# Kernel optimization log

Measured on AMD Instinct MI355X. Metric: run time of the kernel, lower is better.

Reference implementation:

```python
import jax, jax.numpy as jnp
import numpy as np

D_MODEL = 2048
N_HEADS = 16
HEAD_DIM = D_MODEL // N_HEADS


def setup_inputs() -> dict:
    key = jax.random.key(0)
    ks = jax.random.split(key, 5)
    s = 0.02
    return {
        "x": jax.random.normal(ks[0], (4, 2048, D_MODEL), dtype=jnp.float32),
        "w_qkv": jax.random.normal(ks[1], (D_MODEL, 3 * D_MODEL), dtype=jnp.float32) * s,
        "b_qkv": jnp.zeros((3 * D_MODEL,), dtype=jnp.float32),
        "w_out": jax.random.normal(ks[2], (D_MODEL, D_MODEL), dtype=jnp.float32) * s,
        "b_out": jnp.zeros((D_MODEL,), dtype=jnp.float32),
    }


def reference(x, w_qkv, b_qkv, w_out, b_out):
    B, T, C = x.shape
    qkv = x @ w_qkv + b_qkv  # [B,T,3C]
    q, k, v = jnp.split(qkv, 3, axis=-1)
    # [B,T,C] -> [B,H,T,hd]
    def to_heads(t):
        return t.reshape(B, T, N_HEADS, HEAD_DIM).transpose(0, 2, 1, 3)
    q, k, v = to_heads(q), to_heads(k), to_heads(v)
    scale = 1.0 / jnp.sqrt(jnp.asarray(HEAD_DIM, dtype=x.dtype))
    attn = jnp.einsum("bhqd,bhkd->bhqk", q, k) * scale
    causal = jnp.tril(jnp.ones((T, T), dtype=bool))
    attn = jnp.where(causal[None, None], attn, jnp.asarray(-jnp.inf, dtype=attn.dtype))
    attn = jax.nn.softmax(attn, axis=-1)
    out = jnp.einsum("bhqk,bhkd->bhqd", attn, v)
    out = out.transpose(0, 2, 1, 3).reshape(B, T, C)
    return out @ w_out + b_out
```

## Files before the change

### kernel.cpp

```cpp
#include <hip/hip_runtime.h>
#include <hip/hip_bf16.h>

#define DEVFN static __device__ __forceinline__

typedef __attribute__((ext_vector_type(8))) __bf16 bf16x8;
typedef __attribute__((ext_vector_type(4))) float f32x4;

#define MFMA16(a, b, c) __builtin_amdgcn_mfma_f32_16x16x32_bf16(a, b, c, 0, 0, 0)

DEVFN void gload16(const void* g, void* l) {
  __builtin_amdgcn_global_load_lds((const __attribute__((address_space(1))) void*)g,
                                   (__attribute__((address_space(3))) void*)l, 16, 0, 0);
}

DEVFN void vwait8() { asm volatile("s_waitcnt vmcnt(8)" ::: "memory"); __builtin_amdgcn_sched_barrier(0); }
DEVFN void vwait4() { asm volatile("s_waitcnt vmcnt(4)" ::: "memory"); __builtin_amdgcn_sched_barrier(0); }
DEVFN void vwait0() { asm volatile("s_waitcnt vmcnt(0)" ::: "memory"); __builtin_amdgcn_sched_barrier(0); }
DEVFN void bar()    { __builtin_amdgcn_s_barrier(); }
DEVFN void barsched() { __builtin_amdgcn_s_barrier(); __builtin_amdgcn_sched_barrier(0); }

__global__ __launch_bounds__(256) void cvt_f32_bf16(const float* __restrict__ in,
                                                    __bf16* __restrict__ out) {
  size_t i = ((size_t)blockIdx.x * 256 + threadIdx.x) * 8;
  f32x4 a = *(const f32x4*)(in + i);
  f32x4 b = *(const f32x4*)(in + i + 4);
  bf16x8 u;
  u[0] = (__bf16)a[0]; u[1] = (__bf16)a[1]; u[2] = (__bf16)a[2]; u[3] = (__bf16)a[3];
  u[4] = (__bf16)b[0]; u[5] = (__bf16)b[1]; u[6] = (__bf16)b[2]; u[7] = (__bf16)b[3];
  *(bf16x8*)(out + i) = u;
}

__global__ __launch_bounds__(256) void transpose_w(const float* __restrict__ in,
                                                   __bf16* __restrict__ out,
                                                   int K, int N) {
  __shared__ float tile[32][33];
  const int t = threadIdx.x, tx = t & 31, ty = t >> 5;
  const int n0 = blockIdx.x * 32, k0 = blockIdx.y * 32;
#pragma unroll
  for (int r = 0; r < 4; r++)
    tile[ty + r * 8][tx] = in[(size_t)(k0 + ty + r * 8) * N + n0 + tx];
  __syncthreads();
#pragma unroll
  for (int r = 0; r < 4; r++)
    out[(size_t)(n0 + ty + r * 8) * K + k0 + tx] = (__bf16)tile[tx][ty + r * 8];
}

__global__ __launch_bounds__(256) void transpose_v(const __bf16* __restrict__ in,
                                                   __bf16* __restrict__ out) {
  __shared__ __bf16 tile[64][72];
  const int bh = blockIdx.z;
  const int t0 = blockIdx.x * 64, d0 = blockIdx.y * 64;
  const int tid = threadIdx.x;
  const int r = tid >> 3, c8 = (tid & 7) * 8;
  const __bf16* ip = in + (size_t)bh * 2048 * 128;
#pragma unroll
  for (int i = 0; i < 2; i++)
    *(bf16x8*)&tile[i * 32 + r][c8] =
        *(const bf16x8*)(ip + (size_t)(t0 + i * 32 + r) * 128 + d0 + c8);
  __syncthreads();
  __bf16* op = out + (size_t)bh * 2048 * 128;
#pragma unroll
  for (int i = 0; i < 2; i++) {
    const int dd = i * 32 + r;
    bf16x8 v;
#pragma unroll
    for (int j = 0; j < 8; j++) v[j] = tile[c8 + j][dd];
    *(bf16x8*)(op + (size_t)(d0 + dd) * 2048 + t0 + c8) = v;
  }
}

#define QK_SCALE 0.12751745f

DEVFN void stage_tile(const __bf16* gx, size_t Kst, int t, __bf16* ldst,
                      int rr, int gsw, int w) {
#pragma unroll
  for (int j = 0; j < 4; j++)
    gload16(gx + (size_t)(j * 64 + rr) * Kst + (size_t)t * 64 + gsw,
            ldst + j * 4096 + w * 512);
}

DEVFN void stage_chunk(const __bf16* gx, size_t Kst, int t, __bf16* ldst, int j,
                       int rr, int gsw, int w) {
  gload16(gx + (size_t)(j * 64 + rr) * Kst + (size_t)t * 64 + gsw,
          ldst + j * 4096 + w * 512);
}

DEVFN void tile_step(__bf16* la, __bf16* lb, f32x4 (&acc)[8][4],
                     const __bf16* ga, const __bf16* gb, size_t Kst, int t, int NT,
                     int rr, int gsw, int w, int wr, int wc, int lg, int li) {
  bf16x8 a[4][2], bl[2][2], br[2][2];
  const int sa = li & 7;
  const int arow = wr * 128 + li;
  const int brow = wc * 64 + li;
  const bool pf = (t + 2 < NT);

#pragma unroll
  for (int mi = 0; mi < 4; mi++)
#pragma unroll
    for (int ks = 0; ks < 2; ks++)
      a[mi][ks] = *(const bf16x8*)&la[(arow + mi * 16) * 64 + (((ks * 4 + lg) ^ sa) * 8)];
#pragma unroll
  for (int ni = 0; ni < 2; ni++)
#pragma unroll
    for (int ks = 0; ks < 2; ks++)
      bl[ni][ks] = *(const bf16x8*)&lb[(brow + ni * 16) * 64 + (((ks * 4 + lg) ^ sa) * 8)];
  bar();
  __builtin_amdgcn_s_setprio(1);
#pragma unroll
  for (int mi = 0; mi < 4; mi++)
#pragma unroll
    for (int ni = 0; ni < 2; ni++)
#pragma unroll
      for (int ks = 0; ks < 2; ks++)
        acc[mi][ni] = MFMA16(a[mi][ks], bl[ni][ks], acc[mi][ni]);
  __builtin_amdgcn_s_setprio(0);
  barsched();

#pragma unroll
  for (int ni = 0; ni < 2; ni++)
#pragma unroll
    for (int ks = 0; ks < 2; ks++)
      br[ni][ks] = *(const bf16x8*)&lb[(brow + (ni + 2) * 16) * 64 + (((ks * 4 + lg) ^ sa) * 8)];
  if (pf) {
    stage_chunk(ga, Kst, t + 2, la, 0, rr, gsw, w);
    stage_chunk(ga, Kst, t + 2, la, 2, rr, gsw, w);
  }
  bar();
  __builtin_amdgcn_s_setprio(1);
#pragma unroll
  for (int mi = 0; mi < 4; mi++)
#pragma unroll
    for (int ni = 0; ni < 2; ni++)
#pragma unroll
      for (int ks = 0; ks < 2; ks++)
        acc[mi][ni + 2] = MFMA16(a[mi][ks], br[ni][ks], acc[mi][ni + 2]);
  __builtin_amdgcn_s_setprio(0);
  barsched();

#pragma unroll
  for (int mi = 0; mi < 4; mi++)
#pragma unroll
    for (int ks = 0; ks < 2; ks++)
      a[mi][ks] = *(const bf16x8*)&la[(arow + (mi + 4) * 16) * 64 + (((ks * 4 + lg) ^ sa) * 8)];
  if (pf) {
    stage_chunk(gb, Kst, t + 2, lb, 0, rr, gsw, w);
    stage_chunk(gb, Kst, t + 2, lb, 1, rr, gsw, w);
  }
  bar();
  __builtin_amdgcn_s_setprio(1);
#pragma unroll
  for (int mi = 0; mi < 4; mi++)
#pragma unroll
    for (int ni = 0; ni < 2; ni++)
#pragma unroll
      for (int ks = 0; ks < 2; ks++)
        acc[mi + 4][ni] = MFMA16(a[mi][ks], bl[ni][ks], acc[mi + 4][ni]);
  __builtin_amdgcn_s_setprio(0);
  barsched();

  if (pf) {
    stage_chunk(gb, Kst, t + 2, lb, 2, rr, gsw, w);
    stage_chunk(gb, Kst, t + 2, lb, 3, rr, gsw, w);
    stage_chunk(ga, Kst, t + 2, la, 1, rr, gsw, w);
    stage_chunk(ga, Kst, t + 2, la, 3, rr, gsw, w);
  }
  __builtin_amdgcn_s_setprio(1);
#pragma unroll
  for (int mi = 0; mi < 4; mi++)
#pragma unroll
    for (int ni = 0; ni < 2; ni++)
#pragma unroll
      for (int ks = 0; ks < 2; ks++)
        acc[mi + 4][ni + 2] = MFMA16(a[mi][ks], br[ni][ks], acc[mi + 4][ni + 2]);
  __builtin_amdgcn_s_setprio(0);

  if (pf) vwait8(); else vwait0();
  bar();
}

template <int MODE>
__global__ __launch_bounds__(512, 2) void gemm256(
    const __bf16* __restrict__ A, const __bf16* __restrict__ Bt,
    const float* __restrict__ bias, int K, int Ncols,
    __bf16* __restrict__ qo, __bf16* __restrict__ ko, __bf16* __restrict__ vo,
    float* __restrict__ outf) {
  __shared__ __align__(16) __bf16 lds[65536];
  const int tid = threadIdx.x;
  const int w = tid >> 6, lane = tid & 63;
  const int wr = w >> 2, wc = w & 3;
  const int lg = lane >> 4, li = lane & 15;
  const int nbx = gridDim.x;
  const int orig = (int)blockIdx.y * nbx + (int)blockIdx.x;
  const int x = orig & 7, i = orig >> 3;
  const int xc = x & 1, xr = x >> 1;
  const int hw = nbx >> 1;
  const int band = i >> 5;
  const int j = i & 31;
  const size_t n0 = (size_t)(xc * hw + band * 4 + (j & 3)) * 256;
  const size_t m0 = (size_t)(xr * 8 + (j >> 2)) * 256;
  const int rr = tid >> 3;
  const int gsw = ((tid & 7) ^ (rr & 7)) * 8;
  const __bf16* ga = A + m0 * K;
  const __bf16* gb = Bt + n0 * K;
  const int NT = K >> 6;

  __bf16* la0 = lds;
  __bf16* la1 = lds + 16384;
  __bf16* lb0 = lds + 32768;
  __bf16* lb1 = lds + 49152;

  f32x4 acc[8][4] = {};

  stage_tile(ga, K, 0, la0, rr, gsw, w);
  stage_tile(gb, K, 0, lb0, rr, gsw, w);
  stage_tile(ga, K, 1, la1, rr, gsw, w);
  stage_tile(gb, K, 1, lb1, rr, gsw, w);
  vwait8();
  bar();

  for (int t = 0; t < NT; t += 2) {
    tile_step(la0, lb0, acc, ga, gb, K, t,     NT, rr, gsw, w, wr, wc, lg, li);
    tile_step(la1, lb1, acc, ga, gb, K, t + 1, NT, rr, gsw, w, wr, wc, lg, li);
  }

  if (MODE == 0) {
    const int which = (int)(n0 >> 11);
    const int b = (int)(m0 >> 11);
    __bf16* outp = (which == 0) ? qo : ((which == 1) ? ko : vo);
    const float scale = (which == 0) ? QK_SCALE : 1.0f;
#pragma unroll
    for (int ni = 0; ni < 4; ni++) {
      const int ncol = (int)n0 + wc * 64 + ni * 16 + li;
      const float bv = bias[ncol];
      const int h = (ncol & 2047) >> 7;
      const int d = ncol & 127;
      const size_t base = (size_t)(b * 16 + h) * (2048 * 128) + d;
#pragma unroll
      for (int mi = 0; mi < 8; mi++)
#pragma unroll
        for (int r = 0; r < 4; r++) {
          const int tt = ((int)m0 + wr * 128 + mi * 16 + lg * 4 + r) & 2047;
          outp[base + (size_t)tt * 128] = (__bf16)((acc[mi][ni][r] + bv) * scale);
        }
    }
  } else {
#pragma unroll
    for (int ni = 0; ni < 4; ni++) {
      const int ncol = (int)n0 + wc * 64 + ni * 16 + li;
      const float bv = bias[ncol];
#pragma unroll
      for (int mi = 0; mi < 8; mi++)
#pragma unroll
        for (int r = 0; r < 4; r++) {
          const size_t mrow = m0 + wr * 128 + mi * 16 + lg * 4 + r;
          outf[mrow * Ncols + ncol] = acc[mi][ni][r] + bv;
        }
    }
  }
}

DEVFN void attn_stageK(const __bf16* const (&ksrc)[4], int k0, __bf16* Kl, int w) {
#pragma unroll
  for (int i = 0; i < 4; i++)
    gload16(ksrc[i] + (size_t)k0 * 128, Kl + i * 2048 + w * 512);
}
DEVFN void attn_stageV(const __bf16* const (&vsrc)[4], int k0, __bf16* Vl, int w) {
#pragma unroll
  for (int i = 0; i < 4; i++)
    gload16(vsrc[i] + k0, Vl + i * 2048 + w * 512);
}

template <bool DIAG>
DEVFN void attn_tile(int kt, int n, int q0, int w, int lg, int li,
                     const __bf16* const (&ksrc)[4], const __bf16* const (&vsrc)[4],
                     __bf16* Kl, __bf16* Vl, __bf16* Pl,
                     const bf16x8 (&qf)[2][4], f32x4 (&o)[2][8],
                     float (&mrow)[2][4], float (&lrow)[2][4]) {
  const int k0 = kt * 64;
  const bool more = (kt + 1 < n);

  vwait4();
  barsched();

  f32x4 s[2][4] = {};
#pragma unroll
  for (int kk = 0; kk < 4; kk++) {
    bf16x8 bk[4];
#pragma unroll
    for (int ni = 0; ni < 4; ni++) {
      const int key = ni * 16 + li;
      bk[ni] = *(const bf16x8*)&Kl[key * 128 + ((kk * 32 + lg * 8) ^ ((key & 7) << 3))];
    }
#pragma unroll
    for (int mi = 0; mi < 2; mi++)
#pragma unroll
      for (int ni = 0; ni < 4; ni++)
        s[mi][ni] = MFMA16(qf[mi][kk], bk[ni], s[mi][ni]);
  }
  barsched();
  if (more) attn_stageK(ksrc, k0 + 64, Kl, w);

#pragma unroll
  for (int mi = 0; mi < 2; mi++) {
#pragma unroll
    for (int r = 0; r < 4; r++) {
      const int prow = w * 32 + mi * 16 + lg * 4 + r;
      float vals[4];
#pragma unroll
      for (int ni = 0; ni < 4; ni++) {
        float x = s[mi][ni][r];
        if (DIAG) {
          if ((k0 + ni * 16 + li) > (q0 + prow)) x = -1e30f;
        }
        vals[ni] = x;
      }
      float vmax = fmaxf(fmaxf(vals[0], vals[1]), fmaxf(vals[2], vals[3]));
      vmax = fmaxf(vmax, __shfl_xor(vmax, 1));
      vmax = fmaxf(vmax, __shfl_xor(vmax, 2));
      vmax = fmaxf(vmax, __shfl_xor(vmax, 4));
      vmax = fmaxf(vmax, __shfl_xor(vmax, 8));
      float mref = mrow[mi][r];
      if (vmax - mref > 8.0f) {
        const float sc = __builtin_amdgcn_exp2f(mref - vmax);
        lrow[mi][r] *= sc;
#pragma unroll
        for (int nd = 0; nd < 8; nd++) o[mi][nd][r] *= sc;
        mrow[mi][r] = vmax;
        mref = vmax;
      }
      float ps = 0.f;
#pragma unroll
      for (int ni = 0; ni < 4; ni++) {
        const float p = __builtin_amdgcn_exp2f(vals[ni] - mref);
        ps += p;
        Pl[prow * 72 + ni * 16 + li] = (__bf16)p;
      }
      ps += __shfl_xor(ps, 1);
      ps += __shfl_xor(ps, 2);
      ps += __shfl_xor(ps, 4);
      ps += __shfl_xor(ps, 8);
      lrow[mi][r] += ps;
    }
  }

  if (more) vwait4(); else vwait0();
  barsched();

#pragma unroll
  for (int kk = 0; kk < 2; kk++) {
    bf16x8 pf[2];
#pragma unroll
    for (int mi = 0; mi < 2; mi++)
      pf[mi] = *(const bf16x8*)&Pl[(w * 32 + mi * 16 + li) * 72 + kk * 32 + lg * 8];
#pragma unroll
    for (int nd = 0; nd < 8; nd++) {
      const int d = nd * 16 + li;
      const int swd = ((d ^ (d >> 3)) & 7) << 3;
      bf16x8 vf = *(const bf16x8*)&Vl[d * 64 + ((kk * 32 + lg * 8) ^ swd)];
#pragma unroll
      for (int mi = 0; mi < 2; mi++)
        o[mi][nd] = MFMA16(pf[mi], vf, o[mi][nd]);
    }
  }
  barsched();
  if (more) attn_stageV(vsrc, k0 + 64, Vl, w);
}

DEVFN void attn_run(int qt, int bh, int w, int lg, int li,
                    const __bf16* qp, __bf16* ob,
                    const __bf16* const (&ksrc)[4], const __bf16* const (&vsrc)[4],
                    __bf16* Kl, __bf16* Vl, __bf16* Pl) {
  const int q0 = qt * 128;
  bf16x8 qf[2][4];
#pragma unroll
  for (int mi = 0; mi < 2; mi++)
#pragma unroll
    for (int kk = 0; kk < 4; kk++)
      qf[mi][kk] = *(const bf16x8*)(qp + (size_t)(q0 + w * 32 + mi * 16 + li) * 128 + kk * 32 + lg * 8);

  f32x4 o[2][8] = {};
  float mrow[2][4], lrow[2][4];
#pragma unroll
  for (int mi = 0; mi < 2; mi++)
#pragma unroll
    for (int r = 0; r < 4; r++) { mrow[mi][r] = -1e30f; lrow[mi][r] = 0.f; }

  const int n = 2 * qt + 2;
  attn_stageK(ksrc, 0, Kl, w);
  attn_stageV(vsrc, 0, Vl, w);

  for (int kt = 0; kt < n - 2; kt++)
    attn_tile<false>(kt, n, q0, w, lg, li, ksrc, vsrc, Kl, Vl, Pl, qf, o, mrow, lrow);
  attn_tile<true>(n - 2, n, q0, w, lg, li, ksrc, vsrc, Kl, Vl, Pl, qf, o, mrow, lrow);
  attn_tile<true>(n - 1, n, q0, w, lg, li, ksrc, vsrc, Kl, Vl, Pl, qf, o, mrow, lrow);

  const int b = bh >> 4, h = bh & 15;
#pragma unroll
  for (int mi = 0; mi < 2; mi++) {
    float inv[4];
#pragma unroll
    for (int r = 0; r < 4; r++) inv[r] = 1.0f / lrow[mi][r];
#pragma unroll
    for (int nd = 0; nd < 8; nd++)
#pragma unroll
      for (int r = 0; r < 4; r++)
        ob[(size_t)(b * 2048 + q0 + w * 32 + mi * 16 + lg * 4 + r) * 2048 + h * 128 + nd * 16 + li]
            = (__bf16)(o[mi][nd][r] * inv[r]);
  }
}

__global__ __launch_bounds__(256, 2) void attn_fwd(
    const __bf16* __restrict__ qb, const __bf16* __restrict__ kb,
    const __bf16* __restrict__ vtb, __bf16* __restrict__ ob) {
  __shared__ __align__(16) __bf16 Kl[64 * 128];
  __shared__ __align__(16) __bf16 Vl[128 * 64];
  __shared__ __align__(16) __bf16 Pl[128 * 72];
  const int orig = (int)blockIdx.y * 8 + (int)blockIdx.x;
  const int swz = (orig & 7) * 64 + (orig >> 3);
  const int bx = swz & 7;
  const int bh = swz >> 3;
  const int tid = threadIdx.x;
  const int w = tid >> 6, l = tid & 63;
  const int lg = l >> 4, li = l & 15;
  const __bf16* qp = qb + (size_t)bh * (2048 * 128);
  const __bf16* kp = kb + (size_t)bh * (2048 * 128);
  const __bf16* vtp = vtb + (size_t)bh * (2048 * 128);

  const __bf16* ksrc[4];
  const __bf16* vsrc[4];
#pragma unroll
  for (int i = 0; i < 4; i++) {
    const int key = i * 16 + w * 4 + lg;
    ksrc[i] = kp + (size_t)key * 128 + 8 * (li ^ (key & 7));
    const int d = i * 32 + (tid >> 3);
    const int g = (tid & 7) ^ ((d ^ (d >> 3)) & 7);
    vsrc[i] = vtp + (size_t)d * 2048 + g * 8;
  }

  attn_run(15 - bx, bh, w, lg, li, qp, ob, ksrc, vsrc, Kl, Vl, Pl);
  attn_run(bx,      bh, w, lg, li, qp, ob, ksrc, vsrc, Kl, Vl, Pl);
}

extern "C" void kernel_launch(void* const* d_in, const int* in_sizes, int n_in,
                              void* d_out, int out_size, void* d_ws, size_t ws_size,
                              hipStream_t stream) {
  (void)in_sizes; (void)n_in; (void)out_size; (void)ws_size;
  const float* x     = (const float*)d_in[0];
  const float* w_qkv = (const float*)d_in[1];
  const float* b_qkv = (const float*)d_in[2];
  const float* w_out = (const float*)d_in[3];
  const float* b_out = (const float*)d_in[4];
  float* out = (float*)d_out;
  char* ws = (char*)d_ws;

  __bf16* xb    = (__bf16*)(ws + 0);
  __bf16* wqkvT = (__bf16*)(ws + 33554432);
  __bf16* qbuf  = (__bf16*)(ws + 58720256);
  __bf16* kbuf  = (__bf16*)(ws + 92274688);
  __bf16* vbuf  = (__bf16*)(ws + 125829120);
  __bf16* woutT = (__bf16*)(ws + 159383552);

  cvt_f32_bf16<<<8192, 256, 0, stream>>>(x, xb);
  transpose_w<<<dim3(192, 64), 256, 0, stream>>>(w_qkv, wqkvT, 2048, 6144);
  transpose_w<<<dim3(64, 64), 256, 0, stream>>>(w_out, woutT, 2048, 2048);
  gemm256<0><<<dim3(24, 32), 512, 0, stream>>>(xb, wqkvT, b_qkv, 2048, 6144,
                                               qbuf, kbuf, vbuf, nullptr);
  transpose_v<<<dim3(32, 2, 64), 256, 0, stream>>>(vbuf, xb);
  attn_fwd<<<dim3(8, 64), 256, 0, stream>>>(qbuf, kbuf, xb, vbuf);
  gemm256<1><<<dim3(8, 32), 512, 0, stream>>>(vbuf, woutT, b_out, 2048, 2048,
                                              nullptr, nullptr, nullptr, out);
}
```

Measured before the change: 457.6 us.

## Double-buffer K/V tiles in attention and XOR-swizzle the P scratch layout

The attention kernel now keeps two LDS buffers each for K and V. At the start of every key tile it prefetches the next tile's K and V into the spare buffer, instead of restaging into a single buffer in the middle of the tile. This removes two barriers and two waits per tile and gives global loads a full tile of compute to hide behind. The P scratch drops its 72-element padded stride for a 64-wide XOR-swizzled layout. The trade-off is more LDS per block (about 80 KB), which limits occupancy at two blocks per CU.

```diff
diff --git a/kernel.cpp b/kernel.cpp
--- a/kernel.cpp
+++ b/kernel.cpp
@@ -14,7 +14,6 @@
 }
 
 DEVFN void vwait8() { asm volatile("s_waitcnt vmcnt(8)" ::: "memory"); __builtin_amdgcn_sched_barrier(0); }
-DEVFN void vwait4() { asm volatile("s_waitcnt vmcnt(4)" ::: "memory"); __builtin_amdgcn_sched_barrier(0); }
 DEVFN void vwait0() { asm volatile("s_waitcnt vmcnt(0)" ::: "memory"); __builtin_amdgcn_sched_barrier(0); }
 DEVFN void bar()    { __builtin_amdgcn_s_barrier(); }
 DEVFN void barsched() { __builtin_amdgcn_s_barrier(); __builtin_amdgcn_sched_barrier(0); }
@@ -273,13 +272,19 @@
 template <bool DIAG>
 DEVFN void attn_tile(int kt, int n, int q0, int w, int lg, int li,
                      const __bf16* const (&ksrc)[4], const __bf16* const (&vsrc)[4],
-                     __bf16* Kl, __bf16* Vl, __bf16* Pl,
+                     __bf16* Klb, __bf16* Vlb, __bf16* Kln, __bf16* Vln,
+                     __bf16* Pl,
                      const bf16x8 (&qf)[2][4], f32x4 (&o)[2][8],
                      float (&mrow)[2][4], float (&lrow)[2][4]) {
   const int k0 = kt * 64;
-  const bool more = (kt + 1 < n);
-
-  vwait4();
+
+  if (kt + 1 < n) {
+    attn_stageK(ksrc, k0 + 64, Kln, w);
+    attn_stageV(vsrc, k0 + 64, Vln, w);
+    vwait8();
+  } else {
+    vwait0();
+  }
   barsched();
 
   f32x4 s[2][4] = {};
@@ -289,7 +294,7 @@
 #pragma unroll
     for (int ni = 0; ni < 4; ni++) {
       const int key = ni * 16 + li;
-      bk[ni] = *(const bf16x8*)&Kl[key * 128 + ((kk * 32 + lg * 8) ^ ((key & 7) << 3))];
+      bk[ni] = *(const bf16x8*)&Klb[key * 128 + ((kk * 32 + lg * 8) ^ ((key & 7) << 3))];
     }
 #pragma unroll
     for (int mi = 0; mi < 2; mi++)
@@ -297,8 +302,6 @@
       for (int ni = 0; ni < 4; ni++)
         s[mi][ni] = MFMA16(qf[mi][kk], bk[ni], s[mi][ni]);
   }
-  barsched();
-  if (more) attn_stageK(ksrc, k0 + 64, Kl, w);
 
 #pragma unroll
   for (int mi = 0; mi < 2; mi++) {
@@ -329,11 +332,13 @@
         mref = vmax;
       }
       float ps = 0.f;
+      const int rsw = (prow & 7) << 3;
 #pragma unroll
       for (int ni = 0; ni < 4; ni++) {
         const float p = __builtin_amdgcn_exp2f(vals[ni] - mref);
         ps += p;
-        Pl[prow * 72 + ni * 16 + li] = (__bf16)p;
+        const int c = ni * 16 + li;
+        Pl[prow * 64 + (((c & ~7) ^ rsw)) + (c & 7)] = (__bf16)p;
       }
       ps += __shfl_xor(ps, 1);
       ps += __shfl_xor(ps, 2);
@@ -343,33 +348,32 @@
     }
   }
 
-  if (more) vwait4(); else vwait0();
-  barsched();
-
 #pragma unroll
   for (int kk = 0; kk < 2; kk++) {
     bf16x8 pf[2];
 #pragma unroll
-    for (int mi = 0; mi < 2; mi++)
-      pf[mi] = *(const bf16x8*)&Pl[(w * 32 + mi * 16 + li) * 72 + kk * 32 + lg * 8];
+    for (int mi = 0; mi < 2; mi++) {
+      const int pr = w * 32 + mi * 16 + li;
+      pf[mi] = *(const bf16x8*)&Pl[pr * 64 + ((kk * 32 + lg * 8) ^ ((pr & 7) << 3))];
+    }
 #pragma unroll
     for (int nd = 0; nd < 8; nd++) {
       const int d = nd * 16 + li;
       const int swd = ((d ^ (d >> 3)) & 7) << 3;
-      bf16x8 vf = *(const bf16x8*)&Vl[d * 64 + ((kk * 32 + lg * 8) ^ swd)];
+      bf16x8 vf = *(const bf16x8*)&Vlb[d * 64 + ((kk * 32 + lg * 8) ^ swd)];
 #pragma unroll
       for (int mi = 0; mi < 2; mi++)
         o[mi][nd] = MFMA16(pf[mi], vf, o[mi][nd]);
     }
   }
   barsched();
-  if (more) attn_stageV(vsrc, k0 + 64, Vl, w);
 }
 
 DEVFN void attn_run(int qt, int bh, int w, int lg, int li,
                     const __bf16* qp, __bf16* ob,
                     const __bf16* const (&ksrc)[4], const __bf16* const (&vsrc)[4],
-                    __bf16* Kl, __bf16* Vl, __bf16* Pl) {
+                    __bf16* Kl0, __bf16* Kl1, __bf16* Vl0, __bf16* Vl1,
+                    __bf16* Pl) {
   const int q0 = qt * 128;
   bf16x8 qf[2][4];
 #pragma unroll
@@ -386,13 +390,33 @@
     for (int r = 0; r < 4; r++) { mrow[mi][r] = -1e30f; lrow[mi][r] = 0.f; }
 
   const int n = 2 * qt + 2;
-  attn_stageK(ksrc, 0, Kl, w);
-  attn_stageV(vsrc, 0, Vl, w);
-
-  for (int kt = 0; kt < n - 2; kt++)
-    attn_tile<false>(kt, n, q0, w, lg, li, ksrc, vsrc, Kl, Vl, Pl, qf, o, mrow, lrow);
-  attn_tile<true>(n - 2, n, q0, w, lg, li, ksrc, vsrc, Kl, Vl, Pl, qf, o, mrow, lrow);
-  attn_tile<true>(n - 1, n, q0, w, lg, li, ksrc, vsrc, Kl, Vl, Pl, qf, o, mrow, lrow);
+  attn_stageK(ksrc, 0, Kl0, w);
+  attn_stageV(vsrc, 0, Vl0, w);
+
+  for (int kt = 0; kt < n - 2; kt++) {
+    __bf16* kb = (kt & 1) ? Kl1 : Kl0;
+    __bf16* vb = (kt & 1) ? Vl1 : Vl0;
+    __bf16* kn = (kt & 1) ? Kl0 : Kl1;
+    __bf16* vn = (kt & 1) ? Vl0 : Vl1;
+    attn_tile<false>(kt, n, q0, w, lg, li, ksrc, vsrc, kb, vb, kn, vn, Pl,
+                     qf, o, mrow, lrow);
+  }
+  {
+    const int kt = n - 2;
+    __bf16* kb = (kt & 1) ? Kl1 : Kl0;
+    __bf16* vb = (kt & 1) ? Vl1 : Vl0;
+    __bf16* kn = (kt & 1) ? Kl0 : Kl1;
+    __bf16* vn = (kt & 1) ? Vl0 : Vl1;
+    attn_tile<true>(kt, n, q0, w, lg, li, ksrc, vsrc, kb, vb, kn, vn, Pl,
+                    qf, o, mrow, lrow);
+  }
+  {
+    const int kt = n - 1;
+    __bf16* kb = (kt & 1) ? Kl1 : Kl0;
+    __bf16* vb = (kt & 1) ? Vl1 : Vl0;
+    attn_tile<true>(kt, n, q0, w, lg, li, ksrc, vsrc, kb, vb, kb, vb, Pl,
+                    qf, o, mrow, lrow);
+  }
 
   const int b = bh >> 4, h = bh & 15;
 #pragma unroll
@@ -412,9 +436,9 @@
 __global__ __launch_bounds__(256, 2) void attn_fwd(
     const __bf16* __restrict__ qb, const __bf16* __restrict__ kb,
     const __bf16* __restrict__ vtb, __bf16* __restrict__ ob) {
-  __shared__ __align__(16) __bf16 Kl[64 * 128];
-  __shared__ __align__(16) __bf16 Vl[128 * 64];
-  __shared__ __align__(16) __bf16 Pl[128 * 72];
+  __shared__ __align__(16) __bf16 Kl[2][64 * 128];
+  __shared__ __align__(16) __bf16 Vl[2][128 * 64];
+  __shared__ __align__(16) __bf16 Pl[128 * 64];
   const int orig = (int)blockIdx.y * 8 + (int)blockIdx.x;
   const int swz = (orig & 7) * 64 + (orig >> 3);
   const int bx = swz & 7;
@@ -437,8 +461,10 @@
     vsrc[i] = vtp + (size_t)d * 2048 + g * 8;
   }
 
-  attn_run(15 - bx, bh, w, lg, li, qp, ob, ksrc, vsrc, Kl, Vl, Pl);
-  attn_run(bx,      bh, w, lg, li, qp, ob, ksrc, vsrc, Kl, Vl, Pl);
+  attn_run(15 - bx, bh, w, lg, li, qp, ob, ksrc, vsrc,
+           Kl[0], Kl[1], Vl[0], Vl[1], Pl);
+  attn_run(bx,      bh, w, lg, li, qp, ob, ksrc, vsrc,
+           Kl[0], Kl[1], Vl[0], Vl[1], Pl);
 }
 
 extern "C" void kernel_launch(void* const* d_in, const int* in_sizes, int n_in,
```

Result: slower. 488.0 us (+6.6%).

## Switch attention to 32x32 MFMA with transposed scores and register-resident P

Applied to the files above, without the earlier changes.

The attention kernel now computes S^T with 32x32x16 bf16 MFMAs, so each lane holds one query row. That makes the row max and row sum mostly lane-local, needing only one cross-half shuffle each. P is packed to bf16 and exchanged between wave halves with shuffles to form the A operand of the PV MFMA. This removes the P round trip through shared memory and its LDS allocation. The trade-off is extra shuffles to rescale O and more accumulator registers per lane, which may affect occupancy.

```diff
diff --git a/kernel.cpp b/kernel.cpp
--- a/kernel.cpp
+++ b/kernel.cpp
@@ -5,8 +5,10 @@
 
 typedef __attribute__((ext_vector_type(8))) __bf16 bf16x8;
 typedef __attribute__((ext_vector_type(4))) float f32x4;
+typedef __attribute__((ext_vector_type(16))) float f32x16;
 
 #define MFMA16(a, b, c) __builtin_amdgcn_mfma_f32_16x16x32_bf16(a, b, c, 0, 0, 0)
+#define MFMA32(a, b, c) __builtin_amdgcn_mfma_f32_32x32x16_bf16(a, b, c, 0, 0, 0)
 
 DEVFN void gload16(const void* g, void* l) {
   __builtin_amdgcn_global_load_lds((const __attribute__((address_space(1))) void*)g,
@@ -18,6 +20,12 @@
 DEVFN void vwait0() { asm volatile("s_waitcnt vmcnt(0)" ::: "memory"); __builtin_amdgcn_sched_barrier(0); }
 DEVFN void bar()    { __builtin_amdgcn_s_barrier(); }
 DEVFN void barsched() { __builtin_amdgcn_s_barrier(); __builtin_amdgcn_sched_barrier(0); }
+
+DEVFN unsigned pk2(float a, float b) {
+  union { __bf16 h[2]; unsigned u; } z;
+  z.h[0] = (__bf16)a; z.h[1] = (__bf16)b;
+  return z.u;
+}
 
 __global__ __launch_bounds__(256) void cvt_f32_bf16(const float* __restrict__ in,
                                                     __bf16* __restrict__ out) {
@@ -271,142 +279,145 @@
 }
 
 template <bool DIAG>
-DEVFN void attn_tile(int kt, int n, int q0, int w, int lg, int li,
+DEVFN void attn_tile(int kt, int n, int q0w, int w, int lq, int hi,
                      const __bf16* const (&ksrc)[4], const __bf16* const (&vsrc)[4],
-                     __bf16* Kl, __bf16* Vl, __bf16* Pl,
-                     const bf16x8 (&qf)[2][4], f32x4 (&o)[2][8],
-                     float (&mrow)[2][4], float (&lrow)[2][4]) {
+                     __bf16* Kl, __bf16* Vl,
+                     const bf16x8 (&qf)[8], f32x16 (&o)[4],
+                     float& mref, float& lrow) {
   const int k0 = kt * 64;
   const bool more = (kt + 1 < n);
 
   vwait4();
   barsched();
 
-  f32x4 s[2][4] = {};
-#pragma unroll
-  for (int kk = 0; kk < 4; kk++) {
-    bf16x8 bk[4];
-#pragma unroll
-    for (int ni = 0; ni < 4; ni++) {
-      const int key = ni * 16 + li;
-      bk[ni] = *(const bf16x8*)&Kl[key * 128 + ((kk * 32 + lg * 8) ^ ((key & 7) << 3))];
-    }
-#pragma unroll
-    for (int mi = 0; mi < 2; mi++)
-#pragma unroll
-      for (int ni = 0; ni < 4; ni++)
-        s[mi][ni] = MFMA16(qf[mi][kk], bk[ni], s[mi][ni]);
+  f32x16 sT[2];
+  sT[0] = (f32x16)(0.0f); sT[1] = (f32x16)(0.0f);
+#pragma unroll
+  for (int kk = 0; kk < 8; kk++) {
+#pragma unroll
+    for (int nt = 0; nt < 2; nt++) {
+      const int key = nt * 32 + lq;
+      bf16x8 ka = *(const bf16x8*)&Kl[key * 128 + ((kk * 16 + hi * 8) ^ ((key & 7) << 3))];
+      sT[nt] = MFMA32(ka, qf[kk], sT[nt]);
+    }
   }
   barsched();
   if (more) attn_stageK(ksrc, k0 + 64, Kl, w);
 
-#pragma unroll
-  for (int mi = 0; mi < 2; mi++) {
-#pragma unroll
-    for (int r = 0; r < 4; r++) {
-      const int prow = w * 32 + mi * 16 + lg * 4 + r;
-      float vals[4];
-#pragma unroll
-      for (int ni = 0; ni < 4; ni++) {
-        float x = s[mi][ni][r];
-        if (DIAG) {
-          if ((k0 + ni * 16 + li) > (q0 + prow)) x = -1e30f;
-        }
-        vals[ni] = x;
+  float vm0 = -1e30f, vm1 = -1e30f;
+#pragma unroll
+  for (int nt = 0; nt < 2; nt++)
+#pragma unroll
+    for (int r = 0; r < 16; r++) {
+      if (DIAG) {
+        const int key = k0 + nt * 32 + (r & 3) + 8 * (r >> 2) + 4 * hi;
+        if (key > q0w + lq) sT[nt][r] = -1e30f;
       }
-      float vmax = fmaxf(fmaxf(vals[0], vals[1]), fmaxf(vals[2], vals[3]));
-      vmax = fmaxf(vmax, __shfl_xor(vmax, 1));
-      vmax = fmaxf(vmax, __shfl_xor(vmax, 2));
-      vmax = fmaxf(vmax, __shfl_xor(vmax, 4));
-      vmax = fmaxf(vmax, __shfl_xor(vmax, 8));
-      float mref = mrow[mi][r];
-      if (vmax - mref > 8.0f) {
-        const float sc = __builtin_amdgcn_exp2f(mref - vmax);
-        lrow[mi][r] *= sc;
-#pragma unroll
-        for (int nd = 0; nd < 8; nd++) o[mi][nd][r] *= sc;
-        mrow[mi][r] = vmax;
-        mref = vmax;
-      }
-      float ps = 0.f;
-#pragma unroll
-      for (int ni = 0; ni < 4; ni++) {
-        const float p = __builtin_amdgcn_exp2f(vals[ni] - mref);
-        ps += p;
-        Pl[prow * 72 + ni * 16 + li] = (__bf16)p;
-      }
-      ps += __shfl_xor(ps, 1);
-      ps += __shfl_xor(ps, 2);
-      ps += __shfl_xor(ps, 4);
-      ps += __shfl_xor(ps, 8);
-      lrow[mi][r] += ps;
-    }
-  }
+      if (r & 1) vm1 = fmaxf(vm1, sT[nt][r]); else vm0 = fmaxf(vm0, sT[nt][r]);
+    }
+  float vm = fmaxf(vm0, vm1);
+  vm = fmaxf(vm, __shfl_xor(vm, 32));
+
+  if (__any(vm - mref > 8.0f)) {
+    const bool up = vm - mref > 8.0f;
+    const float sc = up ? __builtin_amdgcn_exp2f(mref - vm) : 1.0f;
+    if (up) mref = vm;
+    lrow *= sc;
+#pragma unroll
+    for (int r = 0; r < 16; r++) {
+      const float scr = __shfl(sc, (r & 3) + 8 * (r >> 2) + 4 * hi);
+#pragma unroll
+      for (int dt = 0; dt < 4; dt++) o[dt][r] *= scr;
+    }
+  }
+
+  float p0 = 0.f, p1 = 0.f, p2 = 0.f, p3 = 0.f;
+#pragma unroll
+  for (int nt = 0; nt < 2; nt++)
+#pragma unroll
+    for (int r = 0; r < 16; r++) {
+      const float e = __builtin_amdgcn_exp2f(sT[nt][r] - mref);
+      sT[nt][r] = e;
+      if ((r & 3) == 0) p0 += e; else if ((r & 3) == 1) p1 += e;
+      else if ((r & 3) == 2) p2 += e; else p3 += e;
+    }
+  float ps = (p0 + p1) + (p2 + p3);
+  ps += __shfl_xor(ps, 32);
+  lrow += ps;
+
+  bf16x8 pa[4];
+#pragma unroll
+  for (int nt = 0; nt < 2; nt++)
+#pragma unroll
+    for (int b = 0; b < 2; b++) {
+      const int bs = 8 * b + 4 * hi;
+      const int bc = 8 * b + 4 * (1 - hi);
+      unsigned s0 = pk2(sT[nt][bs + 0], sT[nt][bs + 1]);
+      unsigned s1 = pk2(sT[nt][bs + 2], sT[nt][bs + 3]);
+      unsigned c0 = pk2(sT[nt][bc + 0], sT[nt][bc + 1]);
+      unsigned c1 = pk2(sT[nt][bc + 2], sT[nt][bc + 3]);
+      unsigned r0 = (unsigned)__shfl_xor((int)c0, 32);
+      unsigned r1 = (unsigned)__shfl_xor((int)c1, 32);
+      union { unsigned u[4]; bf16x8 v; } z;
+      if (hi == 0) { z.u[0] = s0; z.u[1] = s1; z.u[2] = r0; z.u[3] = r1; }
+      else         { z.u[0] = r0; z.u[1] = r1; z.u[2] = s0; z.u[3] = s1; }
+      pa[nt * 2 + b] = z.v;
+    }
 
   if (more) vwait4(); else vwait0();
   barsched();
 
 #pragma unroll
-  for (int kk = 0; kk < 2; kk++) {
-    bf16x8 pf[2];
-#pragma unroll
-    for (int mi = 0; mi < 2; mi++)
-      pf[mi] = *(const bf16x8*)&Pl[(w * 32 + mi * 16 + li) * 72 + kk * 32 + lg * 8];
-#pragma unroll
-    for (int nd = 0; nd < 8; nd++) {
-      const int d = nd * 16 + li;
-      const int swd = ((d ^ (d >> 3)) & 7) << 3;
-      bf16x8 vf = *(const bf16x8*)&Vl[d * 64 + ((kk * 32 + lg * 8) ^ swd)];
-#pragma unroll
-      for (int mi = 0; mi < 2; mi++)
-        o[mi][nd] = MFMA16(pf[mi], vf, o[mi][nd]);
-    }
-  }
+  for (int ks = 0; ks < 4; ks++)
+#pragma unroll
+    for (int dt = 0; dt < 4; dt++) {
+      const int d = dt * 32 + lq;
+      bf16x8 vf = *(const bf16x8*)&Vl[d * 64 +
+                     ((ks * 16 + hi * 8) ^ (((d ^ (d >> 3)) & 7) << 3))];
+      o[dt] = MFMA32(pa[ks], vf, o[dt]);
+    }
   barsched();
   if (more) attn_stageV(vsrc, k0 + 64, Vl, w);
 }
 
-DEVFN void attn_run(int qt, int bh, int w, int lg, int li,
+DEVFN void attn_run(int qt, int bh, int w, int lq, int hi,
                     const __bf16* qp, __bf16* ob,
                     const __bf16* const (&ksrc)[4], const __bf16* const (&vsrc)[4],
-                    __bf16* Kl, __bf16* Vl, __bf16* Pl) {
-  const int q0 = qt * 128;
-  bf16x8 qf[2][4];
-#pragma unroll
-  for (int mi = 0; mi < 2; mi++)
-#pragma unroll
-    for (int kk = 0; kk < 4; kk++)
-      qf[mi][kk] = *(const bf16x8*)(qp + (size_t)(q0 + w * 32 + mi * 16 + li) * 128 + kk * 32 + lg * 8);
-
-  f32x4 o[2][8] = {};
-  float mrow[2][4], lrow[2][4];
-#pragma unroll
-  for (int mi = 0; mi < 2; mi++)
-#pragma unroll
-    for (int r = 0; r < 4; r++) { mrow[mi][r] = -1e30f; lrow[mi][r] = 0.f; }
+                    __bf16* Kl, __bf16* Vl) {
+  const int q0w = qt * 128 + w * 32;
+  bf16x8 qf[8];
+#pragma unroll
+  for (int kk = 0; kk < 8; kk++)
+    qf[kk] = *(const bf16x8*)(qp + (size_t)(q0w + lq) * 128 + kk * 16 + hi * 8);
+
+  f32x16 o[4];
+  o[0] = (f32x16)(0.0f); o[1] = (f32x16)(0.0f);
+  o[2] = (f32x16)(0.0f); o[3] = (f32x16)(0.0f);
+  float mref = -1e30f, lrow = 0.f;
 
   const int n = 2 * qt + 2;
   attn_stageK(ksrc, 0, Kl, w);
   attn_stageV(vsrc, 0, Vl, w);
 
   for (int kt = 0; kt < n - 2; kt++)
-    attn_tile<false>(kt, n, q0, w, lg, li, ksrc, vsrc, Kl, Vl, Pl, qf, o, mrow, lrow);
-  attn_tile<true>(n - 2, n, q0, w, lg, li, ksrc, vsrc, Kl, Vl, Pl, qf, o, mrow, lrow);
-  attn_tile<true>(n - 1, n, q0, w, lg, li, ksrc, vsrc, Kl, Vl, Pl, qf, o, mrow, lrow);
+    attn_tile<false>(kt, n, q0w, w, lq, hi, ksrc, vsrc, Kl, Vl, qf, o, mref, lrow);
+  attn_tile<true>(n - 2, n, q0w, w, lq, hi, ksrc, vsrc, Kl, Vl, qf, o, mref, lrow);
+  attn_tile<true>(n - 1, n, q0w, w, lq, hi, ksrc, vsrc, Kl, Vl, qf, o, mref, lrow);
 
   const int b = bh >> 4, h = bh & 15;
-#pragma unroll
-  for (int mi = 0; mi < 2; mi++) {
-    float inv[4];
-#pragma unroll
-    for (int r = 0; r < 4; r++) inv[r] = 1.0f / lrow[mi][r];
-#pragma unroll
-    for (int nd = 0; nd < 8; nd++)
-#pragma unroll
-      for (int r = 0; r < 4; r++)
-        ob[(size_t)(b * 2048 + q0 + w * 32 + mi * 16 + lg * 4 + r) * 2048 + h * 128 + nd * 16 + li]
-            = (__bf16)(o[mi][nd][r] * inv[r]);
-  }
+  const float inv = 1.0f / lrow;
+  float invr[16];
+#pragma unroll
+  for (int r = 0; r < 16; r++)
+    invr[r] = __shfl(inv, (r & 3) + 8 * (r >> 2) + 4 * hi);
+#pragma unroll
+  for (int dt = 0; dt < 4; dt++)
+#pragma unroll
+    for (int r = 0; r < 16; r++) {
+      const int q = q0w + (r & 3) + 8 * (r >> 2) + 4 * hi;
+      ob[(size_t)(b * 2048 + q) * 2048 + h * 128 + dt * 32 + lq]
+          = (__bf16)(o[dt][r] * invr[r]);
+    }
 }
 
 __global__ __launch_bounds__(256, 2) void attn_fwd(
@@ -414,14 +425,14 @@
     const __bf16* __restrict__ vtb, __bf16* __restrict__ ob) {
   __shared__ __align__(16) __bf16 Kl[64 * 128];
   __shared__ __align__(16) __bf16 Vl[128 * 64];
-  __shared__ __align__(16) __bf16 Pl[128 * 72];
   const int orig = (int)blockIdx.y * 8 + (int)blockIdx.x;
   const int swz = (orig & 7) * 64 + (orig >> 3);
   const int bx = swz & 7;
   const int bh = swz >> 3;
   const int tid = threadIdx.x;
   const int w = tid >> 6, l = tid & 63;
-  const int lg = l >> 4, li = l & 15;
+  const int lq = l & 31, hi = l >> 5;
+  const int lg = l >> 4;
   const __bf16* qp = qb + (size_t)bh * (2048 * 128);
   const __bf16* kp = kb + (size_t)bh * (2048 * 128);
   const __bf16* vtp = vtb + (size_t)bh * (2048 * 128);
@@ -431,14 +442,14 @@
 #pragma unroll
   for (int i = 0; i < 4; i++) {
     const int key = i * 16 + w * 4 + lg;
-    ksrc[i] = kp + (size_t)key * 128 + 8 * (li ^ (key & 7));
+    ksrc[i] = kp + (size_t)key * 128 + 8 * ((l & 15) ^ (key & 7));
     const int d = i * 32 + (tid >> 3);
     const int g = (tid & 7) ^ ((d ^ (d >> 3)) & 7);
     vsrc[i] = vtp + (size_t)d * 2048 + g * 8;
   }
 
-  attn_run(15 - bx, bh, w, lg, li, qp, ob, ksrc, vsrc, Kl, Vl, Pl);
-  attn_run(bx,      bh, w, lg, li, qp, ob, ksrc, vsrc, Kl, Vl, Pl);
+  attn_run(15 - bx, bh, w, lq, hi, qp, ob, ksrc, vsrc, Kl, Vl);
+  attn_run(bx,      bh, w, lq, hi, qp, ob, ksrc, vsrc, Kl, Vl);
 }
 
 extern "C" void kernel_launch(void* const* d_in, const int* in_sizes, int n_in,
```

After: 594.8 us. 30.0% more time.
